# Performance work log

Measured on AMD Instinct MI355X. Metric: run time of the kernel, lower is better.

Reference implementation:

```python
import jax, jax.numpy as jnp
import numpy as np

M = 65536  # total flattened feature length (sum of ragged segment lengths n_k)
K = 4096   # number of segments (sub-networks)
B = 256    # batch size


def setup_inputs() -> dict:
    key = jax.random.key(0)
    k1, k2, k3 = jax.random.split(key, 3)
    x = jax.random.normal(k1, (B, 1, M), dtype=jnp.float32)
    w = jax.random.normal(k2, (M,), dtype=jnp.float32)
    # contiguous ragged segments: sorted segment ids in [0, K)
    seg_ids = jnp.sort(jax.random.randint(k3, (M,), 0, K, dtype=jnp.int32))
    return {"x": x, "w": w, "seg_ids": seg_ids, "num_segments": K}


def reference(x, w, seg_ids, num_segments):
    # GINN input layer: for each batch row, slice the flat input into K ragged
    # contiguous segments, dot each segment with the matching slice of the flat
    # weight vector, concatenate the K scalars, apply tanh.
    # Equivalent fused form: u2[b,k] = sum_{i in seg k} w[i]*x[b,0,i]; out = tanh(u2)
    xs = x[:, 0, :]                      # [B, M]
    prod = xs * w                        # [B, M] elementwise
    seg_sum = jax.vmap(
        lambda p: jax.ops.segment_sum(p, seg_ids, num_segments=num_segments)
    )(prod)                              # [B, K]
    return jnp.tanh(seg_sum)
```

## Files before the change

kernel.cpp:

```cpp
#include <hip/hip_runtime.h>


#define TPB 256
#define CH  4608

__global__ void build_seg_ptr(const int* __restrict__ seg_ids,
                              int* __restrict__ seg_ptr,
                              int M, int K) {
    int k = blockIdx.x * blockDim.x + threadIdx.x;
    if (k > K) return;
    int lo = 0, hi = M;
    while (lo < hi) {
        int mid = (lo + hi) >> 1;
        if (seg_ids[mid] < k) lo = mid + 1;
        else hi = mid;
    }
    seg_ptr[k] = lo;
}

__global__ __launch_bounds__(TPB) void seg_reduce_tanh(
        const float* __restrict__ x,
        const float* __restrict__ w,
        const int* __restrict__ seg_ptr,
        float* __restrict__ out,
        int M, int K) {
    __shared__ float prod[CH];

    const int t  = threadIdx.x;
    const int k0 = blockIdx.x * TPB;
    const int b  = blockIdx.y;
    const float* __restrict__ xb = x + (size_t)b * (size_t)M;

    const int s   = seg_ptr[k0];
    const int e   = seg_ptr[k0 + TPB];
    const int a_t = seg_ptr[k0 + t];
    const int b_t = seg_ptr[k0 + t + 1];

    float sum = 0.0f;
    for (int c = s; c < e; c += CH) {
        #pragma unroll
        for (int j = 0; j < CH / TPB; ++j) {
            int m = c + t + j * TPB;
            float v = 0.0f;
            if (m < M) v = xb[m] * w[m];
            prod[t + j * TPB] = v;
        }
        __syncthreads();
        int lo = max(a_t, c);
        int hi = min(b_t, c + CH);
        for (int m = lo; m < hi; ++m) sum += prod[m - c];
        __syncthreads();
    }
    out[(size_t)b * (size_t)K + k0 + t] = tanhf(sum);
}

extern "C" void kernel_launch(void* const* d_in, const int* in_sizes, int n_in,
                              void* d_out, int out_size, void* d_ws, size_t ws_size,
                              hipStream_t stream) {
    const float* x       = (const float*)d_in[0];
    const float* w       = (const float*)d_in[1];
    const int*   seg_ids = (const int*)d_in[2];
    float* out = (float*)d_out;

    const int M = in_sizes[1];
    const int B = in_sizes[0] / M;
    const int K = out_size / B;

    int* seg_ptr = (int*)d_ws;

    build_seg_ptr<<<(K + 1 + 255) / 256, 256, 0, stream>>>(seg_ids, seg_ptr, M, K);

    dim3 grid(K / TPB, B);
    seg_reduce_tanh<<<grid, TPB, 0, stream>>>(x, w, seg_ptr, out, M, K);
}
```

Baseline: 30.74 us.

## Vectorize staging loads with float4 and build segment pointers by scatter

Replaces the per-segment binary search with a per-element scatter that writes segment boundaries directly. Vectorizes the x*w staging into shared memory with aligned float4 loads starting from a 4-aligned base. Enlarges the shared chunk so most blocks finish in a single pass. Loads now stop at e, not M, and rely on c being 4-aligned. The first thread runs a serial loop to fill leading empty segments.

```diff
diff --git a/kernel.cpp b/kernel.cpp
--- a/kernel.cpp
+++ b/kernel.cpp
@@ -2,20 +2,20 @@
 
 
 #define TPB 256
-#define CH  4608
+#define CH  5120
+#define VPT (CH / TPB / 4)
 
-__global__ void build_seg_ptr(const int* __restrict__ seg_ids,
-                              int* __restrict__ seg_ptr,
-                              int M, int K) {
-    int k = blockIdx.x * blockDim.x + threadIdx.x;
-    if (k > K) return;
-    int lo = 0, hi = M;
-    while (lo < hi) {
-        int mid = (lo + hi) >> 1;
-        if (seg_ids[mid] < k) lo = mid + 1;
-        else hi = mid;
+__global__ void build_seg_ptr_scatter(const int* __restrict__ seg_ids,
+                                      int* __restrict__ seg_ptr,
+                                      int M, int K) {
+    int m = blockIdx.x * blockDim.x + threadIdx.x;
+    if (m >= M) return;
+    int a  = seg_ids[m];
+    int nb = (m + 1 < M) ? seg_ids[m + 1] : K;
+    if (m == 0) {
+        for (int k = 0; k <= a; ++k) seg_ptr[k] = 0;
     }
-    seg_ptr[k] = lo;
+    for (int k = a + 1; k <= nb; ++k) seg_ptr[k] = m + 1;
 }
 
 __global__ __launch_bounds__(TPB) void seg_reduce_tanh(
@@ -31,19 +31,29 @@
     const int b  = blockIdx.y;
     const float* __restrict__ xb = x + (size_t)b * (size_t)M;
 
-    const int s   = seg_ptr[k0];
-    const int e   = seg_ptr[k0 + TPB];
-    const int a_t = seg_ptr[k0 + t];
-    const int b_t = seg_ptr[k0 + t + 1];
+    const int s    = seg_ptr[k0];
+    const int e    = seg_ptr[k0 + TPB];
+    const int base = s & ~3;
+    const int a_t  = seg_ptr[k0 + t];
+    const int b_t  = seg_ptr[k0 + t + 1];
 
     float sum = 0.0f;
-    for (int c = s; c < e; c += CH) {
+    for (int c = base; c < e; c += CH) {
+        const float4* __restrict__ x4 = reinterpret_cast<const float4*>(xb + c);
+        const float4* __restrict__ w4 = reinterpret_cast<const float4*>(w + c);
+        float4* __restrict__ p4 = reinterpret_cast<float4*>(prod);
         #pragma unroll
-        for (int j = 0; j < CH / TPB; ++j) {
-            int m = c + t + j * TPB;
-            float v = 0.0f;
-            if (m < M) v = xb[m] * w[m];
-            prod[t + j * TPB] = v;
+        for (int j = 0; j < VPT; ++j) {
+            int idx = t + j * TPB;
+            int mm  = c + idx * 4;
+            float4 v = make_float4(0.f, 0.f, 0.f, 0.f);
+            if (mm < e) {
+                float4 xv = x4[idx];
+                float4 wv = w4[idx];
+                v.x = xv.x * wv.x; v.y = xv.y * wv.y;
+                v.z = xv.z * wv.z; v.w = xv.w * wv.w;
+            }
+            p4[idx] = v;
         }
         __syncthreads();
         int lo = max(a_t, c);
@@ -68,7 +78,7 @@
 
     int* seg_ptr = (int*)d_ws;
 
-    build_seg_ptr<<<(K + 1 + 255) / 256, 256, 0, stream>>>(seg_ids, seg_ptr, M, K);
+    build_seg_ptr_scatter<<<(M + 255) / 256, 256, 0, stream>>>(seg_ids, seg_ptr, M, K);
 
     dim3 grid(K / TPB, B);
     seg_reduce_tanh<<<grid, TPB, 0, stream>>>(x, w, seg_ptr, out, M, K);
```

Measured after the change: 25.64 us. -16.6%, faster.
